# Kernel optimization log

Measured on AMD Instinct MI355X. Metric: run time of the kernel, lower is better.

The kernel has to match this reference:

```python
import jax, jax.numpy as jnp
import numpy as np

B, T, D_IN, E, H = 2, 2048, 1024, 64, 16  # batch, num_tokens, input dim, emb_size(per-head), num_heads


def setup_inputs() -> dict:
    key = jax.random.key(0)
    ks = jax.random.split(key, 6)
    s = 0.02
    inp = jax.random.normal(ks[0], (B, T, D_IN), dtype=jnp.float32)
    # causal mask: 1.0 where attention is disallowed (j > i), matching `scaled_compat -= mask * 1e9`
    mask = jnp.triu(jnp.ones((T, T), dtype=jnp.float32), k=1)
    Wq = jax.random.normal(ks[1], (D_IN, E * H), dtype=jnp.float32) * s
    Wk = jax.random.normal(ks[2], (D_IN, E * H), dtype=jnp.float32) * s
    Wv = jax.random.normal(ks[3], (D_IN, E * H), dtype=jnp.float32) * s
    Wu = jax.random.normal(ks[4], (E * H, E), dtype=jnp.float32) * s
    bu = jnp.zeros((E,), dtype=jnp.float32)
    return {"inp": inp, "mask": mask, "Wq": Wq, "Wk": Wk, "Wv": Wv, "Wu": Wu, "bu": bu}


def reference(inp, mask, Wq, Wk, Wv, Wu, bu):
    b = inp.shape[0]
    q = inp @ Wq  # [B,T,E*H]
    k = inp @ Wk
    v = inp @ Wv
    # NOTE: original reshapes last dim as (E, H) -> heads on fastest axis (interleaved layout)
    q = q.reshape(b, T, E, H)
    k = k.reshape(b, T, E, H)
    v = v.reshape(b, T, E, H)
    scores = jnp.einsum("bteh,bseh->bhts", q, k) / jnp.sqrt(jnp.float32(E))  # [B,H,T,T]
    if mask is not None:
        scores = scores - mask * 1e9
    attn = jax.nn.softmax(scores, axis=-1)
    wv = jnp.einsum("bhts,bseh->bhte", attn, v)  # [B,H,T,E]
    # transpose [0,2,3,1] -> [B,T,E,H], then flatten to [B,T,E*H] (H fastest, matching original)
    wv = jnp.transpose(wv, (0, 2, 3, 1)).reshape(b, T, E * H)
    return wv @ Wu + bu  # unify Dense(emb_size), with bias
```

## Files before the change

### kernel.cpp

```cpp
#include <hip/hip_runtime.h>


typedef __bf16 bf16x8 __attribute__((ext_vector_type(8)));
typedef __bf16 bf16x4 __attribute__((ext_vector_type(4)));
typedef float f32x4 __attribute__((ext_vector_type(4)));
typedef unsigned short u16;
typedef unsigned int u32;

#define AS1 __attribute__((address_space(1)))
#define AS3 __attribute__((address_space(3)))

__device__ __forceinline__ void gll16(const void* g, void* l) {
    __builtin_amdgcn_global_load_lds((const AS1 u32*)g, (AS3 u32*)l, 16, 0, 0);
}

__device__ __forceinline__ u16 f2bf(float f) {
    __bf16 h = (__bf16)f;
    union { __bf16 h; u16 u; } v; v.h = h; return v.u;
}

#define MM 4096
#define SCALE_LOG2E 0.18033688011112042f

__global__ void prep(const float* __restrict__ in, u16* __restrict__ out,
                     const float* __restrict__ Wq, const float* __restrict__ Wk,
                     const float* __restrict__ Wv, const float* __restrict__ Wu,
                     u16* __restrict__ wqt, u16* __restrict__ wkt,
                     u16* __restrict__ wvt, u16* __restrict__ wut) {
    __shared__ float lds[32][33];
    int bid = blockIdx.x, tid = threadIdx.x;
    if (bid < 4096) {
        int i = bid * 256 + tid;
        float4 f = ((const float4*)in)[i];
        bf16x4 o;
        o[0] = (__bf16)f.x; o[1] = (__bf16)f.y; o[2] = (__bf16)f.z; o[3] = (__bf16)f.w;
        ((bf16x4*)out)[i] = o;
        return;
    }
    int bid2 = bid - 4096;
    int z = bid2 >> 10, y = (bid2 >> 5) & 31, x = bid2 & 31;
    const float* src; u16* dst; int N;
    if (z == 0)      { src = Wq; dst = wqt; N = 1024; }
    else if (z == 1) { src = Wk; dst = wkt; N = 1024; }
    else if (z == 2) { src = Wv; dst = wvt; N = 1024; }
    else             { src = Wu; dst = wut; N = 64; if (y >= 2) return; }
    int k0 = x * 32, n0 = y * 32;
    int c = tid & 31, r0 = tid >> 5;
#pragma unroll
    for (int p = 0; p < 4; ++p) {
        int r = r0 + p * 8;
        lds[r][c] = src[(k0 + r) * N + n0 + c];
    }
    __syncthreads();
#pragma unroll
    for (int p = 0; p < 4; ++p) {
        int n = n0 + r0 + p * 8;
        if (z < 3) {
            int rnew = ((n & 15) << 6) | (n >> 4);
            dst[rnew * 1024 + k0 + c] = f2bf(lds[c][n - n0]);
        } else {
            int k = k0 + c;
            int kp = ((k & 15) << 6) | (k >> 4);
            dst[n * 1024 + kp] = f2bf(lds[c][n - n0]);
        }
    }
}

__global__ __launch_bounds__(256) void gemm_qkv(const u16* __restrict__ xb,
                                                const u16* __restrict__ wqt,
                                                const u16* __restrict__ wkt,
                                                const u16* __restrict__ wvt,
                                                u16* __restrict__ qh, u16* __restrict__ kh,
                                                u16* __restrict__ vh) {
    int z = blockIdx.z;
    const u16* wt = (z == 0) ? wqt : (z == 1) ? wkt : wvt;
    u16* dst      = (z == 0) ? qh  : (z == 1) ? kh  : vh;
    __shared__ u16 lA[3][128 * 32];
    __shared__ u16 lB[3][128 * 32];
    int tid = threadIdx.x;
    int m0 = blockIdx.x * 128, n0 = blockIdx.y * 128;
    int lane = tid & 63, w = tid >> 6;
    int wr = w >> 1, wc = w & 1;
    int l15 = lane & 15, quad = lane >> 4;
    f32x4 acc[4][4] = {};
    int srow = tid >> 2, scol = (tid & 3) * 8;
    const u16* ga = xb + (m0 + srow) * 1024 + scol;
    const u16* gb = wt + (n0 + srow) * 1024 + scol;
#pragma unroll
    for (int t0 = 0; t0 < 2; ++t0)
#pragma unroll
        for (int pp = 0; pp < 2; ++pp) {
            gll16(ga + pp * 65536 + t0 * 32, lA[t0] + (pp * 256 + tid) * 8);
            gll16(gb + pp * 65536 + t0 * 32, lB[t0] + (pp * 256 + tid) * 8);
        }
    int cur = 0;
#pragma unroll 1
    for (int kk = 0; kk < 32; ++kk) {
        if (kk < 31) asm volatile("s_waitcnt vmcnt(4)" ::: "memory");
        else         asm volatile("s_waitcnt vmcnt(0)" ::: "memory");
        __builtin_amdgcn_s_barrier();
        if (kk + 2 < 32) {
            int nxt = cur + 2; if (nxt >= 3) nxt -= 3;
            int kb = (kk + 2) * 32;
#pragma unroll
            for (int pp = 0; pp < 2; ++pp) {
                gll16(ga + pp * 65536 + kb, lA[nxt] + (pp * 256 + tid) * 8);
                gll16(gb + pp * 65536 + kb, lB[nxt] + (pp * 256 + tid) * 8);
            }
        }
        bf16x8 af[4], bfr[4];
#pragma unroll
        for (int i = 0; i < 4; ++i)
            af[i] = *(const bf16x8*)(lA[cur] + (wr * 64 + i * 16 + l15) * 32 + quad * 8);
#pragma unroll
        for (int j = 0; j < 4; ++j)
            bfr[j] = *(const bf16x8*)(lB[cur] + (wc * 64 + j * 16 + l15) * 32 + quad * 8);
#pragma unroll
        for (int i = 0; i < 4; ++i)
#pragma unroll
            for (int j = 0; j < 4; ++j)
                acc[i][j] = __builtin_amdgcn_mfma_f32_16x16x32_bf16(af[i], bfr[j], acc[i][j], 0, 0, 0);
        ++cur; if (cur == 3) cur = 0;
    }
    int bb = m0 >> 11;
    int hb = (n0 >> 6) + wc;
    if (z < 2) {
        float scale = (z == 0) ? SCALE_LOG2E : 1.f;
#pragma unroll
        for (int i = 0; i < 4; ++i)
#pragma unroll
            for (int r = 0; r < 4; ++r) {
                int m = m0 + wr * 64 + i * 16 + quad * 4 + r;
                bf16x4 o;
                o[0] = (__bf16)(acc[i][0][r] * scale); o[1] = (__bf16)(acc[i][1][r] * scale);
                o[2] = (__bf16)(acc[i][2][r] * scale); o[3] = (__bf16)(acc[i][3][r] * scale);
                *(bf16x4*)(dst + m * 1024 + hb * 64 + l15 * 4) = o;
            }
    } else {
#pragma unroll
        for (int j = 0; j < 4; ++j)
#pragma unroll
            for (int r = 0; r < 4; ++r) {
                bf16x4 o;
                o[0] = (__bf16)acc[0][j][r]; o[1] = (__bf16)acc[1][j][r];
                o[2] = (__bf16)acc[2][j][r]; o[3] = (__bf16)acc[3][j][r];
                *(bf16x4*)(dst + (((bb * 16 + hb) * 64) + j * 16 + l15) * 2048 +
                           (m0 & 2047) + wr * 64 + (quad * 4 + r) * 4) = o;
            }
    }
}

__global__ __launch_bounds__(256) void attn(const u16* __restrict__ qh, const u16* __restrict__ kh,
                                            const u16* __restrict__ vh, u16* __restrict__ ot,
                                            float* __restrict__ part, float* __restrict__ lp) {
    __shared__ u16 smem[25600];
    u16* sPQ = smem;
    const int tid = threadIdx.x;
    const int lane = tid & 63, w = tid >> 6;
    const int quad = lane >> 4, l15 = lane & 15;
    const int s = blockIdx.x, by = blockIdx.y;
    int qt, j0, j1, half;
    if (s < 8)       { qt = 7 - s;  j0 = 0;      j1 = 2 * qt + 2; half = -1; }
    else if (s < 16) { qt = s;      j0 = 0;      j1 = qt + 1;     half = 0;  }
    else             { qt = s - 8;  j0 = qt + 1; j1 = 2 * qt + 2; half = 1;  }
    const int b = by >> 4, h = by & 15;
    const int row0 = tid >> 3;
    const int cb0 = (tid & 7) ^ (row0 & 7);
    const u16* kg0 = kh + (b * 2048) * 1024 + h * 64 + row0 * 1024 + cb0 * 8;
    const u16* vg0 = vh + (by * 64) * 2048 + row0 * 2048 + cb0 * 8;
    const int fsw = (l15 & 7) * 8;

    const u16* qg = qh + (b * 2048 + qt * 128) * 1024 + h * 64;
#pragma unroll
    for (int p = 0; p < 4; ++p) {
        int c = p * 256 + tid;
        gll16(qg + (c >> 3) * 1024 + (c & 7) * 8, sPQ + c * 8);
    }
    __syncthreads();
    bf16x8 aq[2][2];
#pragma unroll
    for (int rg = 0; rg < 2; ++rg)
#pragma unroll
        for (int k2 = 0; k2 < 2; ++k2)
            aq[rg][k2] = *(const bf16x8*)(sPQ + (w * 32 + rg * 16 + l15) * 64 + k2 * 32 + quad * 8);

    {
        u16* sK0 = smem + 9216;
        u16* sV0 = smem + 17408;
        gll16(kg0 + j0 * 65536,         sK0 + tid * 8);
        gll16(kg0 + j0 * 65536 + 32768, sK0 + (256 + tid) * 8);
        gll16(vg0 + j0 * 64,            sV0 + tid * 8);
        gll16(vg0 + j0 * 64 + 65536,    sV0 + (256 + tid) * 8);
    }
    float lpart[2][4] = {};
    f32x4 oacc[2][4] = {};
    u16* sPw = sPQ + w * 2304;
    for (int jt = j0; jt < j1; ++jt) {
        int cur = (jt - j0) & 1;
        u16* sK = smem + 9216 + cur * 4096;
        u16* sV = smem + 17408 + cur * 4096;
        asm volatile("s_waitcnt vmcnt(0)" ::: "memory");
        __builtin_amdgcn_s_barrier();
        if (jt + 1 < j1) {
            u16* sKn = smem + 9216 + (cur ^ 1) * 4096;
            u16* sVn = smem + 17408 + (cur ^ 1) * 4096;
            gll16(kg0 + (jt + 1) * 65536,         sKn + tid * 8);
            gll16(kg0 + (jt + 1) * 65536 + 32768, sKn + (256 + tid) * 8);
            gll16(vg0 + (jt + 1) * 64,            sVn + tid * 8);
            gll16(vg0 + (jt + 1) * 64 + 65536,    sVn + (256 + tid) * 8);
        }
        f32x4 sacc[2][4] = {};
        __builtin_amdgcn_s_setprio(1);
#pragma unroll
        for (int j4 = 0; j4 < 4; ++j4)
#pragma unroll
            for (int k2 = 0; k2 < 2; ++k2) {
                bf16x8 bk = *(const bf16x8*)(sK + (j4 * 16 + l15) * 64 + (((k2 * 4 + quad) * 8) ^ fsw));
                sacc[0][j4] = __builtin_amdgcn_mfma_f32_16x16x32_bf16(aq[0][k2], bk, sacc[0][j4], 0, 0, 0);
                sacc[1][j4] = __builtin_amdgcn_mfma_f32_16x16x32_bf16(aq[1][k2], bk, sacc[1][j4], 0, 0, 0);
            }
        __builtin_amdgcn_s_setprio(0);
        if (jt >= 2 * qt) {
            int soff = (jt - 2 * qt) * 64;
#pragma unroll
            for (int rg = 0; rg < 2; ++rg)
#pragma unroll
                for (int j4 = 0; j4 < 4; ++j4)
#pragma unroll
                    for (int r = 0; r < 4; ++r) {
                        int sg = soff + j4 * 16 + l15;
                        int tg = w * 32 + rg * 16 + quad * 4 + r;
                        if (sg > tg) sacc[rg][j4][r] = -1e30f;
                    }
        }
#pragma unroll
        for (int rg = 0; rg < 2; ++rg)
#pragma unroll
            for (int r = 0; r < 4; ++r) {
                float p0 = __builtin_amdgcn_exp2f(sacc[rg][0][r]);
                float p1 = __builtin_amdgcn_exp2f(sacc[rg][1][r]);
                float p2 = __builtin_amdgcn_exp2f(sacc[rg][2][r]);
                float p3 = __builtin_amdgcn_exp2f(sacc[rg][3][r]);
                lpart[rg][r] += (p0 + p1) + (p2 + p3);
                bf16x4 o;
                o[0] = (__bf16)p0; o[1] = (__bf16)p1; o[2] = (__bf16)p2; o[3] = (__bf16)p3;
                *(bf16x4*)(sPw + (rg * 16 + quad * 4 + r) * 72 + l15 * 4) = o;
            }
        bf16x8 ap[2][2];
#pragma unroll
        for (int rg = 0; rg < 2; ++rg)
#pragma unroll
            for (int k2 = 0; k2 < 2; ++k2)
                ap[rg][k2] = *(const bf16x8*)(sPw + (rg * 16 + l15) * 72 + k2 * 32 + quad * 8);
        __builtin_amdgcn_s_setprio(1);
#pragma unroll
        for (int e4 = 0; e4 < 4; ++e4)
#pragma unroll
            for (int k2 = 0; k2 < 2; ++k2) {
                bf16x8 bv = *(const bf16x8*)(sV + (e4 * 16 + l15) * 64 + (((k2 * 4 + quad) * 8) ^ fsw));
                oacc[0][e4] = __builtin_amdgcn_mfma_f32_16x16x32_bf16(ap[0][k2], bv, oacc[0][e4], 0, 0, 0);
                oacc[1][e4] = __builtin_amdgcn_mfma_f32_16x16x32_bf16(ap[1][k2], bv, oacc[1][e4], 0, 0, 0);
            }
        __builtin_amdgcn_s_setprio(0);
    }
    if (half < 0) {
#pragma unroll
        for (int rg = 0; rg < 2; ++rg)
#pragma unroll
            for (int r = 0; r < 4; ++r) {
                float rs = lpart[rg][r];
#pragma unroll
                for (int off = 1; off < 16; off <<= 1) rs += __shfl_xor(rs, off, 16);
                float inv = 1.f / rs;
                int t = qt * 128 + w * 32 + rg * 16 + quad * 4 + r;
                int base = (b * 2048 + t) * 1024 + h * 64;
#pragma unroll
                for (int e4 = 0; e4 < 4; ++e4)
                    ot[base + e4 * 16 + l15] = f2bf(oacc[rg][e4][r] * inv);
            }
    } else {
        int pb = by * 8 + (qt - 8);
        float* pg = part + (pb * 2 + half) * 8192;
        float* lg = lp + pb * 256 + half * 128;
#pragma unroll
        for (int rg = 0; rg < 2; ++rg)
#pragma unroll
            for (int r = 0; r < 4; ++r) {
                float rs = lpart[rg][r];
#pragma unroll
                for (int off = 1; off < 16; off <<= 1) rs += __shfl_xor(rs, off, 16);
                int row = w * 32 + rg * 16 + quad * 4 + r;
                if (l15 == 0) lg[row] = rs;
#pragma unroll
                for (int e4 = 0; e4 < 4; ++e4)
                    pg[row * 64 + e4 * 16 + l15] = oacc[rg][e4][r];
            }
    }
}

__global__ __launch_bounds__(256) void combine_o(const float* __restrict__ part,
                                                 const float* __restrict__ lp,
                                                 u16* __restrict__ ot) {
    int pb = blockIdx.x, tid = threadIdx.x;
    int by = pb >> 3, qt = 8 + (pb & 7);
    int b = by >> 4, h = by & 15;
    const float* pA = part + pb * 16384;
    const float* pB = pA + 8192;
    const float* lA = lp + pb * 256;
    const float* lB = lA + 128;
#pragma unroll
    for (int p = 0; p < 8; ++p) {
        int e = p * 1024 + tid * 4;
        int row = e >> 6, col = e & 63;
        float4 a = *(const float4*)(pA + e);
        float4 c = *(const float4*)(pB + e);
        float inv = 1.f / (lA[row] + lB[row]);
        int t = qt * 128 + row;
        bf16x4 o;
        o[0] = (__bf16)((a.x + c.x) * inv); o[1] = (__bf16)((a.y + c.y) * inv);
        o[2] = (__bf16)((a.z + c.z) * inv); o[3] = (__bf16)((a.w + c.w) * inv);
        *(bf16x4*)(ot + (b * 2048 + t) * 1024 + h * 64 + col) = o;
    }
}

__global__ __launch_bounds__(256) void gemm_out(const u16* __restrict__ ot, const u16* __restrict__ wut,
                                                const float* __restrict__ bu, float* __restrict__ out) {
    __shared__ float red[4][1088];
    int tid = threadIdx.x, lane = tid & 63, w = tid >> 6;
    int quad = lane >> 4, l15 = lane & 15;
    int m0 = blockIdx.x * 16;
    f32x4 acc[4] = {};
    const u16* aptr = ot + (m0 + l15) * 1024 + w * 256 + quad * 8;
    const u16* bptr = wut + l15 * 1024 + w * 256 + quad * 8;
#pragma unroll
    for (int kk = 0; kk < 8; ++kk) {
        bf16x8 af = *(const bf16x8*)(aptr + kk * 32);
#pragma unroll
        for (int j = 0; j < 4; ++j) {
            bf16x8 bfr = *(const bf16x8*)(bptr + j * 16 * 1024 + kk * 32);
            acc[j] = __builtin_amdgcn_mfma_f32_16x16x32_bf16(af, bfr, acc[j], 0, 0, 0);
        }
    }
#pragma unroll
    for (int j = 0; j < 4; ++j)
#pragma unroll
        for (int r = 0; r < 4; ++r)
            red[w][(j * 16 + l15) * 17 + quad * 4 + r] = acc[j][r];
    __syncthreads();
    int n = tid & 63, mq = tid >> 6;
    float bias = bu[n];
#pragma unroll
    for (int i = 0; i < 4; ++i) {
        int m = mq * 4 + i;
        float s = red[0][n * 17 + m] + red[1][n * 17 + m] + red[2][n * 17 + m] + red[3][n * 17 + m];
        out[(m0 + m) * 64 + n] = s + bias;
    }
}

#define OFF_XB   0u
#define OFF_WQT  8388608u
#define OFF_WKT  10485760u
#define OFF_WVT  12582912u
#define OFF_WUT  14680064u
#define OFF_QH   14811136u
#define OFF_KH   23199744u
#define OFF_VH   31588352u
#define OFF_OT   OFF_XB
#define OFF_PART 39976960u
#define OFF_LP   56754176u

extern "C" void kernel_launch(void* const* d_in, const int* in_sizes, int n_in,
                              void* d_out, int out_size, void* d_ws, size_t ws_size,
                              hipStream_t stream) {
    (void)in_sizes; (void)n_in; (void)out_size; (void)ws_size;
    const float* inp = (const float*)d_in[0];
    const float* Wq = (const float*)d_in[2];
    const float* Wk = (const float*)d_in[3];
    const float* Wv = (const float*)d_in[4];
    const float* Wu = (const float*)d_in[5];
    const float* bu = (const float*)d_in[6];
    float* out = (float*)d_out;
    char* ws = (char*)d_ws;
    u16* xb  = (u16*)(ws + OFF_XB);
    u16* wqt = (u16*)(ws + OFF_WQT);
    u16* wkt = (u16*)(ws + OFF_WKT);
    u16* wvt = (u16*)(ws + OFF_WVT);
    u16* wut = (u16*)(ws + OFF_WUT);
    u16* qh  = (u16*)(ws + OFF_QH);
    u16* kh  = (u16*)(ws + OFF_KH);
    u16* vh  = (u16*)(ws + OFF_VH);
    u16* ot  = (u16*)(ws + OFF_OT);
    float* part = (float*)(ws + OFF_PART);
    float* lpw  = (float*)(ws + OFF_LP);

    prep<<<8192, 256, 0, stream>>>(inp, xb, Wq, Wk, Wv, Wu, wqt, wkt, wvt, wut);
    gemm_qkv<<<dim3(32, 8, 3), 256, 0, stream>>>(xb, wqt, wkt, wvt, qh, kh, vh);
    attn<<<dim3(24, 32), 256, 0, stream>>>(qh, kh, vh, ot, part, lpw);
    combine_o<<<256, 256, 0, stream>>>(part, lpw, ot);
    gemm_out<<<256, 256, 0, stream>>>(ot, wut, bu, out);
}
```

Measured before the change: 162.7 us.

## Swizzle QKV GEMM LDS layout and fuse split-KV combine into output GEMM

The QKV GEMM now XOR-swizzles the column chunk of each row when writing to LDS and applies the matching swizzle on fragment reads, to reduce LDS bank conflicts. The separate combine_o kernel is removed. gemm_out now reads the two fp32 partial outputs and their row sums directly for the later query tiles, normalizes them and converts to bf16 in registers before the MFMA. This saves one kernel launch and a bf16 round trip through global memory, at the cost of uncoalesced fp32 loads inside gemm_out.

```diff
diff --git a/kernel.cpp b/kernel.cpp
--- a/kernel.cpp
+++ b/kernel.cpp
@@ -83,9 +83,11 @@
     int wr = w >> 1, wc = w & 1;
     int l15 = lane & 15, quad = lane >> 4;
     f32x4 acc[4][4] = {};
-    int srow = tid >> 2, scol = (tid & 3) * 8;
-    const u16* ga = xb + (m0 + srow) * 1024 + scol;
-    const u16* gb = wt + (n0 + srow) * 1024 + scol;
+    int srow = tid >> 2;
+    int scolx = ((tid & 3) * 8) ^ (((srow >> 1) & 3) << 3);
+    const int qsw = (quad ^ ((l15 >> 1) & 3)) * 8;
+    const u16* ga = xb + (m0 + srow) * 1024 + scolx;
+    const u16* gb = wt + (n0 + srow) * 1024 + scolx;
 #pragma unroll
     for (int t0 = 0; t0 < 2; ++t0)
 #pragma unroll
@@ -111,10 +113,10 @@
         bf16x8 af[4], bfr[4];
 #pragma unroll
         for (int i = 0; i < 4; ++i)
-            af[i] = *(const bf16x8*)(lA[cur] + (wr * 64 + i * 16 + l15) * 32 + quad * 8);
+            af[i] = *(const bf16x8*)(lA[cur] + (wr * 64 + i * 16 + l15) * 32 + qsw);
 #pragma unroll
         for (int j = 0; j < 4; ++j)
-            bfr[j] = *(const bf16x8*)(lB[cur] + (wc * 64 + j * 16 + l15) * 32 + quad * 8);
+            bfr[j] = *(const bf16x8*)(lB[cur] + (wc * 64 + j * 16 + l15) * 32 + qsw);
 #pragma unroll
         for (int i = 0; i < 4; ++i)
 #pragma unroll
@@ -298,47 +300,58 @@
     }
 }
 
-__global__ __launch_bounds__(256) void combine_o(const float* __restrict__ part,
-                                                 const float* __restrict__ lp,
-                                                 u16* __restrict__ ot) {
-    int pb = blockIdx.x, tid = threadIdx.x;
-    int by = pb >> 3, qt = 8 + (pb & 7);
-    int b = by >> 4, h = by & 15;
-    const float* pA = part + pb * 16384;
-    const float* pB = pA + 8192;
-    const float* lA = lp + pb * 256;
-    const float* lB = lA + 128;
-#pragma unroll
-    for (int p = 0; p < 8; ++p) {
-        int e = p * 1024 + tid * 4;
-        int row = e >> 6, col = e & 63;
-        float4 a = *(const float4*)(pA + e);
-        float4 c = *(const float4*)(pB + e);
-        float inv = 1.f / (lA[row] + lB[row]);
-        int t = qt * 128 + row;
-        bf16x4 o;
-        o[0] = (__bf16)((a.x + c.x) * inv); o[1] = (__bf16)((a.y + c.y) * inv);
-        o[2] = (__bf16)((a.z + c.z) * inv); o[3] = (__bf16)((a.w + c.w) * inv);
-        *(bf16x4*)(ot + (b * 2048 + t) * 1024 + h * 64 + col) = o;
-    }
-}
-
-__global__ __launch_bounds__(256) void gemm_out(const u16* __restrict__ ot, const u16* __restrict__ wut,
+__global__ __launch_bounds__(256) void gemm_out(const u16* __restrict__ ot,
+                                                const float* __restrict__ part,
+                                                const float* __restrict__ lp,
+                                                const u16* __restrict__ wut,
                                                 const float* __restrict__ bu, float* __restrict__ out) {
     __shared__ float red[4][1088];
     int tid = threadIdx.x, lane = tid & 63, w = tid >> 6;
     int quad = lane >> 4, l15 = lane & 15;
     int m0 = blockIdx.x * 16;
+    int b = m0 >> 11, t0 = m0 & 2047, qt = t0 >> 7;
     f32x4 acc[4] = {};
-    const u16* aptr = ot + (m0 + l15) * 1024 + w * 256 + quad * 8;
     const u16* bptr = wut + l15 * 1024 + w * 256 + quad * 8;
-#pragma unroll
-    for (int kk = 0; kk < 8; ++kk) {
-        bf16x8 af = *(const bf16x8*)(aptr + kk * 32);
-#pragma unroll
-        for (int j = 0; j < 4; ++j) {
-            bf16x8 bfr = *(const bf16x8*)(bptr + j * 16 * 1024 + kk * 32);
-            acc[j] = __builtin_amdgcn_mfma_f32_16x16x32_bf16(af, bfr, acc[j], 0, 0, 0);
+    if (qt < 8) {
+        const u16* aptr = ot + (m0 + l15) * 1024 + w * 256 + quad * 8;
+#pragma unroll
+        for (int kk = 0; kk < 8; ++kk) {
+            bf16x8 af = *(const bf16x8*)(aptr + kk * 32);
+#pragma unroll
+            for (int j = 0; j < 4; ++j) {
+                bf16x8 bfr = *(const bf16x8*)(bptr + j * 16 * 1024 + kk * 32);
+                acc[j] = __builtin_amdgcn_mfma_f32_16x16x32_bf16(af, bfr, acc[j], 0, 0, 0);
+            }
+        }
+    } else {
+        int rowp = (t0 & 127) + l15;
+        float inv4[4];
+#pragma unroll
+        for (int hh = 0; hh < 4; ++hh) {
+            int pb = (b * 16 + w * 4 + hh) * 8 + (qt - 8);
+            inv4[hh] = 1.f / (lp[pb * 256 + rowp] + lp[pb * 256 + 128 + rowp]);
+        }
+#pragma unroll
+        for (int kk = 0; kk < 8; ++kk) {
+            const int hh = kk >> 1;
+            int pb = (b * 16 + w * 4 + hh) * 8 + (qt - 8);
+            int e = (kk & 1) * 32 + quad * 8;
+            const float* pA = part + pb * 16384 + rowp * 64 + e;
+            float4 a0 = *(const float4*)(pA);
+            float4 a1 = *(const float4*)(pA + 4);
+            float4 c0 = *(const float4*)(pA + 8192);
+            float4 c1 = *(const float4*)(pA + 8192 + 4);
+            float inv = inv4[hh];
+            bf16x8 af;
+            af[0] = (__bf16)((a0.x + c0.x) * inv); af[1] = (__bf16)((a0.y + c0.y) * inv);
+            af[2] = (__bf16)((a0.z + c0.z) * inv); af[3] = (__bf16)((a0.w + c0.w) * inv);
+            af[4] = (__bf16)((a1.x + c1.x) * inv); af[5] = (__bf16)((a1.y + c1.y) * inv);
+            af[6] = (__bf16)((a1.z + c1.z) * inv); af[7] = (__bf16)((a1.w + c1.w) * inv);
+#pragma unroll
+            for (int j = 0; j < 4; ++j) {
+                bf16x8 bfr = *(const bf16x8*)(bptr + j * 16 * 1024 + kk * 32);
+                acc[j] = __builtin_amdgcn_mfma_f32_16x16x32_bf16(af, bfr, acc[j], 0, 0, 0);
+            }
         }
     }
 #pragma unroll
@@ -396,6 +409,5 @@
     prep<<<8192, 256, 0, stream>>>(inp, xb, Wq, Wk, Wv, Wu, wqt, wkt, wvt, wut);
     gemm_qkv<<<dim3(32, 8, 3), 256, 0, stream>>>(xb, wqt, wkt, wvt, qh, kh, vh);
     attn<<<dim3(24, 32), 256, 0, stream>>>(qh, kh, vh, ot, part, lpw);
-    combine_o<<<256, 256, 0, stream>>>(part, lpw, ot);
-    gemm_out<<<256, 256, 0, stream>>>(ot, wut, bu, out);
-}
+    gemm_out<<<256, 256, 0, stream>>>(ot, part, lpw, wut, bu, out);
+}
```

Measured after the change: 161.4 us. About the same (-0.8%).
